# Optimization experiments

Hardware: AMD Instinct MI355X
Metric: run time of the kernel (lower is better)

Reference implementation:

```python
import jax, jax.numpy as jnp
import numpy as np

N = 100000      # nodes
E = 1600000     # edges (avg degree 16)
DIN, DH, DOUT = 32, 48, 16


def _glorot(key, fan_in, fan_out):
    s = np.sqrt(6.0 / (fan_in + fan_out)).astype(np.float32)
    return jax.random.uniform(key, (fan_in, fan_out), jnp.float32, -s, s)


def setup_inputs() -> dict:
    key = jax.random.key(0)
    ks = jax.random.split(key, 6)
    x = jax.random.normal(ks[0], (N, DIN), jnp.float32)
    edge_index = jax.random.randint(ks[1], (2, E), 0, N, jnp.int32)
    return {
        "x": x,
        "edge_index": edge_index,
        "W1": _glorot(ks[2], DIN, DH), "b1": jnp.zeros((DH,), jnp.float32),
        "W2": _glorot(ks[3], DH, DH),  "b2": jnp.zeros((DH,), jnp.float32),
        "W3": _glorot(ks[4], DH, DOUT), "b3": jnp.zeros((DOUT,), jnp.float32),
    }


def reference(x, edge_index, W1, b1, W2, b2, W3, b3):
    # GCNConv with add_self_loops=True and symmetric normalization (gcn_norm).
    src, dst = edge_index[0], edge_index[1]
    loops = jnp.arange(N, dtype=src.dtype)
    src = jnp.concatenate([src, loops])  # [E+N]
    dst = jnp.concatenate([dst, loops])
    # in-degree at targets (edge weights are all ones)
    deg = jax.ops.segment_sum(jnp.ones(src.shape[0], jnp.float32), dst, num_segments=N)
    dinv = jnp.where(deg > 0, jax.lax.rsqrt(deg), 0.0)
    norm = dinv[src] * dinv[dst]  # [E+N]

    def conv(h, W, b):
        h = h @ W                          # [N, d_out] per-node linear
        m = h[src] * norm[:, None]         # gather + scale messages
        return jax.ops.segment_sum(m, dst, num_segments=N) + b  # scatter-add

    h = jax.nn.relu(conv(x, W1, b1))
    h = jax.nn.relu(conv(h, W2, b2))
    return conv(h, W3, b3)
```

## Files before the change

### kernel.cpp

```cpp
#include <hip/hip_runtime.h>
#include <hip/hip_fp16.h>


constexpr int Nn   = 100000;
constexpr int Ne   = 1600000;
constexpr int DIN  = 32;
constexpr int DH   = 48;
constexpr int DOUT = 16;
constexpr int TPB  = 256;

constexpr int BSH   = 7;
constexpr int NPBK  = 1 << BSH;
constexpr int NBUK  = (Nn + NPBK - 1) / NPBK;
constexpr int CAP   = 2560;
constexpr int EPB   = 4096;
constexpr int NBLKA = (Ne + EPB - 1) / EPB;

static inline int cdiv(long long a, long long b){ return (int)((a+b-1)/b); }
__device__ inline float4 ld4(const float* p){ return *reinterpret_cast<const float4*>(p); }

__device__ inline void ld8h(const __half* p, float* v){
    union { float4 f; __half2 h[4]; } u;
    u.f = *reinterpret_cast<const float4*>(p);
#pragma unroll
    for (int q = 0; q < 4; ++q) {
        float2 t = __half22float2(u.h[q]);
        v[2*q] = t.x; v[2*q+1] = t.y;
    }
}


__global__ __launch_bounds__(1024) void initA_k(int* __restrict__ cursorA){
    int t = threadIdx.x;
    if (t < NBUK) cursorA[t] = t * CAP;
}

__global__ __launch_bounds__(TPB) void passA_k(const int* __restrict__ src,
                                               const int* __restrict__ dst,
                                               int* __restrict__ cursorA,
                                               int2* __restrict__ tmp){
    __shared__ int hist[NBUK];
    __shared__ int cbase[NBUK];
    const int t = threadIdx.x;
    for (int i = t; i < NBUK; i += TPB) hist[i] = 0;
    __syncthreads();
    const int e0 = blockIdx.x * EPB;
    const int e1 = min(e0 + EPB, Ne);
    for (int k = 0; k < EPB / (TPB * 4); ++k) {
        int e = e0 + k * (TPB * 4) + t * 4;
        if (e + 3 < e1) {
            int4 d4 = *reinterpret_cast<const int4*>(dst + e);
            atomicAdd(&hist[d4.x >> BSH], 1);
            atomicAdd(&hist[d4.y >> BSH], 1);
            atomicAdd(&hist[d4.z >> BSH], 1);
            atomicAdd(&hist[d4.w >> BSH], 1);
        } else {
            for (int j = 0; j < 4; ++j) { int ee = e + j; if (ee < e1) atomicAdd(&hist[dst[ee] >> BSH], 1); }
        }
    }
    __syncthreads();
    for (int b = t; b < NBUK; b += TPB) {
        int c = hist[b];
        cbase[b] = c ? atomicAdd(&cursorA[b], c) : 0;
        hist[b] = 0;
    }
    __syncthreads();
    for (int k = 0; k < EPB / (TPB * 4); ++k) {
        int e = e0 + k * (TPB * 4) + t * 4;
        if (e + 3 < e1) {
            int4 s4 = *reinterpret_cast<const int4*>(src + e);
            int4 d4 = *reinterpret_cast<const int4*>(dst + e);
            int b0 = d4.x >> BSH, b1 = d4.y >> BSH, b2 = d4.z >> BSH, b3 = d4.w >> BSH;
            int p0 = cbase[b0] + atomicAdd(&hist[b0], 1);
            int p1 = cbase[b1] + atomicAdd(&hist[b1], 1);
            int p2 = cbase[b2] + atomicAdd(&hist[b2], 1);
            int p3 = cbase[b3] + atomicAdd(&hist[b3], 1);
            if (p0 < (b0 + 1) * CAP) tmp[p0] = make_int2(s4.x, d4.x);
            if (p1 < (b1 + 1) * CAP) tmp[p1] = make_int2(s4.y, d4.y);
            if (p2 < (b2 + 1) * CAP) tmp[p2] = make_int2(s4.z, d4.z);
            if (p3 < (b3 + 1) * CAP) tmp[p3] = make_int2(s4.w, d4.w);
        } else {
            for (int j = 0; j < 4; ++j) {
                int ee = e + j;
                if (ee < e1) {
                    int s = src[ee], d = dst[ee];
                    int bb = d >> BSH;
                    int p = cbase[bb] + atomicAdd(&hist[bb], 1);
                    if (p < (bb + 1) * CAP) tmp[p] = make_int2(s, d);
                }
            }
        }
    }
}

__global__ __launch_bounds__(1024) void bucket_scan_k(const int* __restrict__ cursorA,
                                                      int* __restrict__ bucket_base,
                                                      int* __restrict__ rpN){
    __shared__ int s[1024];
    int t = threadIdx.x;
    int tot = (t < NBUK) ? (cursorA[t] - t * CAP) : 0;
    s[t] = tot;
    __syncthreads();
    for (int off = 1; off < 1024; off <<= 1) {
        int u = (t >= off) ? s[t - off] : 0;
        __syncthreads();
        s[t] += u;
        __syncthreads();
    }
    if (t < NBUK) bucket_base[t] = s[t] - tot;
    if (t == NBUK - 1) { bucket_base[NBUK] = s[t]; rpN[Nn] = s[t]; }
}

__global__ __launch_bounds__(TPB) void passB_k(const int2* __restrict__ tmp,
                                               const int* __restrict__ cursorA,
                                               const int* __restrict__ bucket_base,
                                               int* __restrict__ rpN,
                                               float* __restrict__ dinv,
                                               int* __restrict__ csr_src){
    __shared__ int ncnt[NPBK];
    __shared__ int s[NPBK];
    __shared__ int ncur[NPBK];
    const int t = threadIdx.x;
    const int b = blockIdx.x;
    const int e0 = b * CAP;
    const int e1 = min(cursorA[b], (b + 1) * CAP);
    const int cnt = e1 - e0;
    if (t < NPBK) ncnt[t] = 0;
    __syncthreads();
    for (int k = t; k < cnt; k += TPB) {
        int2 ed = tmp[e0 + k];
        atomicAdd(&ncnt[ed.y & (NPBK - 1)], 1);
    }
    __syncthreads();
    int my = 0;
    if (t < NPBK) { my = ncnt[t]; s[t] = my; }
    __syncthreads();
    for (int off = 1; off < NPBK; off <<= 1) {
        int u = 0;
        if (t < NPBK && t >= off) u = s[t - off];
        __syncthreads();
        if (t < NPBK) s[t] += u;
        __syncthreads();
    }
    if (t < NPBK) {
        int goff = bucket_base[b] + s[t] - my;
        ncur[t] = goff;
        int node = (b << BSH) + t;
        if (node < Nn) { rpN[node] = goff; dinv[node] = rsqrtf(1.0f + (float)my); }
    }
    __syncthreads();
    for (int k = t; k < cnt; k += TPB) {
        int2 ed = tmp[e0 + k];
        int pos = atomicAdd(&ncur[ed.y & (NPBK - 1)], 1);
        csr_src[pos] = ed.x;
    }
}

__global__ __launch_bounds__(TPB) void conv_x_k(const float* __restrict__ x,
                                                const float* __restrict__ dinv,
                                                __half* __restrict__ xh){
    int g = blockIdx.x * TPB + threadIdx.x;
    if (g >= Nn * (DIN / 8)) return;
    int i  = g / (DIN / 8);
    int j8 = (g % (DIN / 8)) * 8;
    float dn = dinv[i];
    float4 a = ld4(x + (size_t)i * DIN + j8);
    float4 c = ld4(x + (size_t)i * DIN + j8 + 4);
    union { float4 f; __half2 h[4]; } u;
    u.h[0] = __floats2half2_rn(a.x * dn, a.y * dn);
    u.h[1] = __floats2half2_rn(a.z * dn, a.w * dn);
    u.h[2] = __floats2half2_rn(c.x * dn, c.y * dn);
    u.h[3] = __floats2half2_rn(c.z * dn, c.w * dn);
    *reinterpret_cast<float4*>(xh + (size_t)i * DIN + j8) = u.f;
}

template <int D, int G, bool BIAS>
__global__ __launch_bounds__(TPB) void gather_h_k(const __half* __restrict__ tab,
                                                  const int* __restrict__ rpN,
                                                  const int* __restrict__ csr_src,
                                                  const float* __restrict__ dinv,
                                                  const float* __restrict__ b,
                                                  float* __restrict__ out){
    constexpr int NPB = TPB / G;
    const int local = threadIdx.x / G;
    const int f8    = threadIdx.x % G;
    if (local >= NPB) return;
    const int i = blockIdx.x * NPB + local;
    if (i >= Nn) return;

    const int hoff = f8 * 8;
    float acc[8];
    ld8h(tab + (size_t)i * D + hoff, acc);

    const int beg = rpN[i];
    const int end = rpN[i + 1];
    int k = beg;
    float v0[8], v1[8];
    for (; k + 1 < end; k += 2) {
        int s0 = csr_src[k];
        int s1 = csr_src[k + 1];
        ld8h(tab + (size_t)s0 * D + hoff, v0);
        ld8h(tab + (size_t)s1 * D + hoff, v1);
#pragma unroll
        for (int q = 0; q < 8; ++q) acc[q] += v0[q] + v1[q];
    }
    if (k < end) {
        int s0 = csr_src[k];
        ld8h(tab + (size_t)s0 * D + hoff, v0);
#pragma unroll
        for (int q = 0; q < 8; ++q) acc[q] += v0[q];
    }

    const float dn = dinv[i];
    float o[8];
    if (BIAS) {
        float4 ba = ld4(b + hoff);
        float4 bc = ld4(b + hoff + 4);
        o[0]=acc[0]*dn+ba.x; o[1]=acc[1]*dn+ba.y; o[2]=acc[2]*dn+ba.z; o[3]=acc[3]*dn+ba.w;
        o[4]=acc[4]*dn+bc.x; o[5]=acc[5]*dn+bc.y; o[6]=acc[6]*dn+bc.z; o[7]=acc[7]*dn+bc.w;
    } else {
#pragma unroll
        for (int q = 0; q < 8; ++q) o[q] = acc[q] * dn;
    }
    float* op = out + (size_t)i * D + hoff;
    *reinterpret_cast<float4*>(op)     = make_float4(o[0], o[1], o[2], o[3]);
    *reinterpret_cast<float4*>(op + 4) = make_float4(o[4], o[5], o[6], o[7]);
}

__global__ __launch_bounds__(TPB) void linear12_k(const float* __restrict__ agg,
                                                  const float* __restrict__ W1,
                                                  const float* __restrict__ b1,
                                                  const float* __restrict__ W2,
                                                  const float* __restrict__ dinv,
                                                  __half* __restrict__ t2h) {
    constexpr int PAD = DIN + 1;
    __shared__ float sW1[DIN * DH];
    __shared__ float sW2[DH * DH];
    __shared__ float sb1[DH];
    __shared__ float sh[TPB * PAD];
    const int t = threadIdx.x;
    const int base = blockIdx.x * TPB;

    for (int i = t; i < DIN * DH; i += TPB) sW1[i] = W1[i];
    for (int i = t; i < DH * DH; i += TPB) sW2[i] = W2[i];
    if (t < DH) sb1[t] = b1[t];
    for (int idx = t; idx < TPB * DIN; idx += TPB) {
        int g = base * DIN + idx;
        float v = (g < Nn * DIN) ? agg[g] : 0.0f;
        sh[(idx / DIN) * PAD + (idx % DIN)] = v;
    }
    __syncthreads();

    const int node = base + t;
    if (node >= Nn) return;

    float h1[DH];
#pragma unroll
    for (int j = 0; j < DH; ++j) h1[j] = sb1[j];
    for (int k = 0; k < DIN; ++k) {
        float a = sh[t * PAD + k];
#pragma unroll
        for (int j = 0; j < DH; ++j) h1[j] += a * sW1[k * DH + j];
    }
#pragma unroll
    for (int j = 0; j < DH; ++j) h1[j] = fmaxf(h1[j], 0.0f);

    float o[DH];
#pragma unroll
    for (int j = 0; j < DH; ++j) o[j] = 0.0f;
    for (int k = 0; k < DH; ++k) {
        float a = h1[k];
#pragma unroll
        for (int j = 0; j < DH; ++j) o[j] += a * sW2[k * DH + j];
    }
    const float dn = dinv[node];
    __half2* tp = reinterpret_cast<__half2*>(t2h + (size_t)node * DH);
#pragma unroll
    for (int j = 0; j < DH / 2; ++j)
        tp[j] = __floats2half2_rn(o[2*j] * dn, o[2*j+1] * dn);
}

__global__ __launch_bounds__(TPB) void linear3_k(const float* __restrict__ h,
                                                 const float* __restrict__ W,
                                                 const float* __restrict__ dinv,
                                                 __half* __restrict__ t3h) {
    constexpr int PAD = DH + 1;
    __shared__ float sW[DH * DOUT];
    __shared__ float sh[TPB * PAD];
    const int base = blockIdx.x * TPB;

    for (int idx = threadIdx.x; idx < DH * DOUT; idx += TPB) sW[idx] = W[idx];
    for (int idx = threadIdx.x; idx < TPB * DH; idx += TPB) {
        int g = base * DH + idx;
        float v = (g < Nn * DH) ? h[g] : 0.0f;
        sh[(idx / DH) * PAD + (idx % DH)] = fmaxf(v, 0.0f);
    }
    __syncthreads();

    const int node = base + threadIdx.x;
    if (node >= Nn) return;

    float acc[DOUT];
#pragma unroll
    for (int j = 0; j < DOUT; ++j) acc[j] = 0.0f;
    for (int k = 0; k < DH; ++k) {
        float a = sh[threadIdx.x * PAD + k];
#pragma unroll
        for (int j = 0; j < DOUT; ++j) acc[j] += a * sW[k * DOUT + j];
    }
    float dn = dinv[node];
    __half2* tp = reinterpret_cast<__half2*>(t3h + (size_t)node * DOUT);
#pragma unroll
    for (int j = 0; j < DOUT / 2; ++j)
        tp[j] = __floats2half2_rn(acc[2*j] * dn, acc[2*j+1] * dn);
}


extern "C" void kernel_launch(void* const* d_in, const int* in_sizes, int n_in,
                              void* d_out, int out_size, void* d_ws, size_t ws_size,
                              hipStream_t stream) {
    const float* x  = (const float*)d_in[0];
    const int*   ei = (const int*)d_in[1];
    const float* W1 = (const float*)d_in[2];
    const float* b1 = (const float*)d_in[3];
    const float* W2 = (const float*)d_in[4];
    const float* b2 = (const float*)d_in[5];
    const float* W3 = (const float*)d_in[6];
    const float* b3 = (const float*)d_in[7];
    const int* src = ei;
    const int* dst = ei + Ne;

    char* w = (char*)d_ws;
    int*   cursorA     = (int*)w;   w += 1024 * 4;
    int*   bucket_base = (int*)w;   w += 1024 * 4;
    int*   rpN         = (int*)w;   w += 100608L * 4;
    float* dinv        = (float*)w; w += 100352L * 4;
    int*   csr_src     = (int*)w;   w += 1600512L * 4;
    float* bufA        = (float*)w; w += (size_t)Nn * DH * 4;
    float* bufB        = (float*)w;
    int2*   tmp   = (int2*)bufA;
    __half* xh    = (__half*)bufA;
    __half* t2h   = (__half*)bufA;
    __half* t3h   = (__half*)bufA;
    float*  agg32 = bufB;
    float*  h2    = bufB;
    float*  out   = (float*)d_out;

    initA_k<<<1, 1024, 0, stream>>>(cursorA);
    passA_k<<<NBLKA, TPB, 0, stream>>>(src, dst, cursorA, tmp);
    bucket_scan_k<<<1, 1024, 0, stream>>>(cursorA, bucket_base, rpN);
    passB_k<<<NBUK, TPB, 0, stream>>>(tmp, cursorA, bucket_base, rpN, dinv, csr_src);

    conv_x_k<<<cdiv((long long)Nn * (DIN / 8), TPB), TPB, 0, stream>>>(x, dinv, xh);
    gather_h_k<DIN, DIN/8, false><<<cdiv(Nn, TPB/(DIN/8)), TPB, 0, stream>>>(xh, rpN, csr_src, dinv, nullptr, agg32);
    linear12_k<<<cdiv(Nn, TPB), TPB, 0, stream>>>(agg32, W1, b1, W2, dinv, t2h);

    gather_h_k<DH, DH/8, true><<<cdiv(Nn, TPB/(DH/8)), TPB, 0, stream>>>(t2h, rpN, csr_src, dinv, b2, h2);

    linear3_k<<<cdiv(Nn, TPB), TPB, 0, stream>>>(h2, W3, dinv, t3h);
    gather_h_k<DOUT, DOUT/8, true><<<cdiv(Nn, TPB/(DOUT/8)), TPB, 0, stream>>>(t3h, rpN, csr_src, dinv, b3, out);
}
```

Measured before the change: 265.1 us.

## Enlarge CSR buckets, fuse x-scaling into passB, unroll gather by four

Widens destination buckets from 128 to 512 nodes, so there are 196 buckets, with larger per-bucket capacity and edges per passA block. The scan kernels shrink to 256 threads and passB runs one thread per node. The separate conv_x kernel is folded into passB, which scales x by dinv and converts it to half right after building the CSR rows. xh moves into bufB so it no longer aliases the tmp buffer that passB still reads. The gather loop is unrolled to four neighbours per iteration for more memory-level parallelism, at the cost of more registers and a scalar remainder loop.

```diff
diff --git a/kernel.cpp b/kernel.cpp
--- a/kernel.cpp
+++ b/kernel.cpp
@@ -9,11 +9,11 @@
 constexpr int DOUT = 16;
 constexpr int TPB  = 256;
 
-constexpr int BSH   = 7;
+constexpr int BSH   = 9;
 constexpr int NPBK  = 1 << BSH;
 constexpr int NBUK  = (Nn + NPBK - 1) / NPBK;
-constexpr int CAP   = 2560;
-constexpr int EPB   = 4096;
+constexpr int CAP   = 9216;
+constexpr int EPB   = 8192;
 constexpr int NBLKA = (Ne + EPB - 1) / EPB;
 
 static inline int cdiv(long long a, long long b){ return (int)((a+b-1)/b); }
@@ -30,7 +30,7 @@
 }
 
 
-__global__ __launch_bounds__(1024) void initA_k(int* __restrict__ cursorA){
+__global__ __launch_bounds__(256) void initA_k(int* __restrict__ cursorA){
     int t = threadIdx.x;
     if (t < NBUK) cursorA[t] = t * CAP;
 }
@@ -93,15 +93,15 @@
     }
 }
 
-__global__ __launch_bounds__(1024) void bucket_scan_k(const int* __restrict__ cursorA,
-                                                      int* __restrict__ bucket_base,
-                                                      int* __restrict__ rpN){
-    __shared__ int s[1024];
+__global__ __launch_bounds__(256) void bucket_scan_k(const int* __restrict__ cursorA,
+                                                     int* __restrict__ bucket_base,
+                                                     int* __restrict__ rpN){
+    __shared__ int s[256];
     int t = threadIdx.x;
     int tot = (t < NBUK) ? (cursorA[t] - t * CAP) : 0;
     s[t] = tot;
     __syncthreads();
-    for (int off = 1; off < 1024; off <<= 1) {
+    for (int off = 1; off < 256; off <<= 1) {
         int u = (t >= off) ? s[t - off] : 0;
         __syncthreads();
         s[t] += u;
@@ -111,12 +111,14 @@
     if (t == NBUK - 1) { bucket_base[NBUK] = s[t]; rpN[Nn] = s[t]; }
 }
 
-__global__ __launch_bounds__(TPB) void passB_k(const int2* __restrict__ tmp,
-                                               const int* __restrict__ cursorA,
-                                               const int* __restrict__ bucket_base,
-                                               int* __restrict__ rpN,
-                                               float* __restrict__ dinv,
-                                               int* __restrict__ csr_src){
+__global__ __launch_bounds__(NPBK) void passB_k(const int2* __restrict__ tmp,
+                                                const int* __restrict__ cursorA,
+                                                const int* __restrict__ bucket_base,
+                                                int* __restrict__ rpN,
+                                                float* __restrict__ dinv,
+                                                int* __restrict__ csr_src,
+                                                const float* __restrict__ x,
+                                                __half* __restrict__ xh){
     __shared__ int ncnt[NPBK];
     __shared__ int s[NPBK];
     __shared__ int ncur[NPBK];
@@ -125,53 +127,51 @@
     const int e0 = b * CAP;
     const int e1 = min(cursorA[b], (b + 1) * CAP);
     const int cnt = e1 - e0;
-    if (t < NPBK) ncnt[t] = 0;
-    __syncthreads();
-    for (int k = t; k < cnt; k += TPB) {
+    ncnt[t] = 0;
+    __syncthreads();
+    for (int k = t; k < cnt; k += NPBK) {
         int2 ed = tmp[e0 + k];
         atomicAdd(&ncnt[ed.y & (NPBK - 1)], 1);
     }
     __syncthreads();
-    int my = 0;
-    if (t < NPBK) { my = ncnt[t]; s[t] = my; }
+    int my = ncnt[t];
+    s[t] = my;
     __syncthreads();
     for (int off = 1; off < NPBK; off <<= 1) {
-        int u = 0;
-        if (t < NPBK && t >= off) u = s[t - off];
+        int u = (t >= off) ? s[t - off] : 0;
         __syncthreads();
-        if (t < NPBK) s[t] += u;
+        s[t] += u;
         __syncthreads();
     }
-    if (t < NPBK) {
-        int goff = bucket_base[b] + s[t] - my;
-        ncur[t] = goff;
-        int node = (b << BSH) + t;
-        if (node < Nn) { rpN[node] = goff; dinv[node] = rsqrtf(1.0f + (float)my); }
-    }
-    __syncthreads();
-    for (int k = t; k < cnt; k += TPB) {
+    int goff = bucket_base[b] + s[t] - my;
+    ncur[t] = goff;
+    const int node = (b << BSH) + t;
+    const float dn = rsqrtf(1.0f + (float)my);
+    if (node < Nn) {
+        rpN[node] = goff;
+        dinv[node] = dn;
+    }
+    __syncthreads();
+    for (int k = t; k < cnt; k += NPBK) {
         int2 ed = tmp[e0 + k];
         int pos = atomicAdd(&ncur[ed.y & (NPBK - 1)], 1);
         csr_src[pos] = ed.x;
     }
-}
-
-__global__ __launch_bounds__(TPB) void conv_x_k(const float* __restrict__ x,
-                                                const float* __restrict__ dinv,
-                                                __half* __restrict__ xh){
-    int g = blockIdx.x * TPB + threadIdx.x;
-    if (g >= Nn * (DIN / 8)) return;
-    int i  = g / (DIN / 8);
-    int j8 = (g % (DIN / 8)) * 8;
-    float dn = dinv[i];
-    float4 a = ld4(x + (size_t)i * DIN + j8);
-    float4 c = ld4(x + (size_t)i * DIN + j8 + 4);
-    union { float4 f; __half2 h[4]; } u;
-    u.h[0] = __floats2half2_rn(a.x * dn, a.y * dn);
-    u.h[1] = __floats2half2_rn(a.z * dn, a.w * dn);
-    u.h[2] = __floats2half2_rn(c.x * dn, c.y * dn);
-    u.h[3] = __floats2half2_rn(c.z * dn, c.w * dn);
-    *reinterpret_cast<float4*>(xh + (size_t)i * DIN + j8) = u.f;
+    if (node < Nn) {
+        const float* xp = x + (size_t)node * DIN;
+        __half* xhp = xh + (size_t)node * DIN;
+#pragma unroll
+        for (int q = 0; q < DIN / 8; ++q) {
+            float4 a = ld4(xp + q * 8);
+            float4 c = ld4(xp + q * 8 + 4);
+            union { float4 f; __half2 h[4]; } u;
+            u.h[0] = __floats2half2_rn(a.x * dn, a.y * dn);
+            u.h[1] = __floats2half2_rn(a.z * dn, a.w * dn);
+            u.h[2] = __floats2half2_rn(c.x * dn, c.y * dn);
+            u.h[3] = __floats2half2_rn(c.z * dn, c.w * dn);
+            *reinterpret_cast<float4*>(xhp + q * 8) = u.f;
+        }
+    }
 }
 
 template <int D, int G, bool BIAS>
@@ -195,16 +195,20 @@
     const int beg = rpN[i];
     const int end = rpN[i + 1];
     int k = beg;
-    float v0[8], v1[8];
-    for (; k + 1 < end; k += 2) {
+    float v0[8], v1[8], v2[8], v3[8];
+    for (; k + 3 < end; k += 4) {
         int s0 = csr_src[k];
         int s1 = csr_src[k + 1];
+        int s2 = csr_src[k + 2];
+        int s3 = csr_src[k + 3];
         ld8h(tab + (size_t)s0 * D + hoff, v0);
         ld8h(tab + (size_t)s1 * D + hoff, v1);
-#pragma unroll
-        for (int q = 0; q < 8; ++q) acc[q] += v0[q] + v1[q];
-    }
-    if (k < end) {
+        ld8h(tab + (size_t)s2 * D + hoff, v2);
+        ld8h(tab + (size_t)s3 * D + hoff, v3);
+#pragma unroll
+        for (int q = 0; q < 8; ++q) acc[q] += (v0[q] + v1[q]) + (v2[q] + v3[q]);
+    }
+    for (; k < end; ++k) {
         int s0 = csr_src[k];
         ld8h(tab + (size_t)s0 * D + hoff, v0);
 #pragma unroll
@@ -339,19 +343,18 @@
     float* bufA        = (float*)w; w += (size_t)Nn * DH * 4;
     float* bufB        = (float*)w;
     int2*   tmp   = (int2*)bufA;
-    __half* xh    = (__half*)bufA;
     __half* t2h   = (__half*)bufA;
     __half* t3h   = (__half*)bufA;
     float*  agg32 = bufB;
+    __half* xh    = (__half*)((char*)bufB + (size_t)Nn * DIN * 4);
     float*  h2    = bufB;
     float*  out   = (float*)d_out;
 
-    initA_k<<<1, 1024, 0, stream>>>(cursorA);
+    initA_k<<<1, 256, 0, stream>>>(cursorA);
     passA_k<<<NBLKA, TPB, 0, stream>>>(src, dst, cursorA, tmp);
-    bucket_scan_k<<<1, 1024, 0, stream>>>(cursorA, bucket_base, rpN);
-    passB_k<<<NBUK, TPB, 0, stream>>>(tmp, cursorA, bucket_base, rpN, dinv, csr_src);
-
-    conv_x_k<<<cdiv((long long)Nn * (DIN / 8), TPB), TPB, 0, stream>>>(x, dinv, xh);
+    bucket_scan_k<<<1, 256, 0, stream>>>(cursorA, bucket_base, rpN);
+    passB_k<<<NBUK, NPBK, 0, stream>>>(tmp, cursorA, bucket_base, rpN, dinv, csr_src, x, xh);
+
     gather_h_k<DIN, DIN/8, false><<<cdiv(Nn, TPB/(DIN/8)), TPB, 0, stream>>>(xh, rpN, csr_src, dinv, nullptr, agg32);
     linear12_k<<<cdiv(Nn, TPB), TPB, 0, stream>>>(agg32, W1, b1, W2, dinv, t2h);
 
```

After: 248.2 us. 6.4% less time.
